# Performance work log

Hardware: AMD Instinct MI355X
Metric: run time of the kernel (lower is better)

## Reference

```python
import jax, jax.numpy as jnp
import numpy as np

N_NODES = 50000
IN_CH = 128
OUT_CH = 64
N_EDGES = 800000
K_HOPS = 2


def setup_inputs() -> dict:
    key = jax.random.key(0)
    k1, k2, k3, k4 = jax.random.split(key, 4)
    x = jax.random.normal(k1, (N_NODES, IN_CH), dtype=jnp.float32)
    edge_index = jax.random.randint(k2, (2, N_EDGES), 0, N_NODES, dtype=jnp.int64)
    # SGC linear layer params (torch Linear default init approx)
    scale = 1.0 / np.sqrt(IN_CH)
    W = jax.random.uniform(k3, (IN_CH, OUT_CH), dtype=jnp.float32, minval=-scale, maxval=scale)
    b = jax.random.uniform(k4, (OUT_CH,), dtype=jnp.float32, minval=-scale, maxval=scale)
    return {"x": x, "edge_index": edge_index, "W": W, "b": b}


def _sgc_propagate(x, row, col, K):
    # GCN symmetric normalization with self-loops: S = D^-1/2 (A+I) D^-1/2
    n = x.shape[0]
    loop = jnp.arange(n, dtype=row.dtype)
    row = jnp.concatenate([row, loop])
    col = jnp.concatenate([col, loop])
    ones = jnp.ones(row.shape[0], dtype=x.dtype)
    deg = jax.ops.segment_sum(ones, col, num_segments=n)
    dinv = jnp.where(deg > 0, jax.lax.rsqrt(deg), 0.0)
    norm = dinv[row] * dinv[col]  # [E+N]
    for _ in range(K):
        # gather source features, weight, scatter-add to targets
        msg = norm[:, None] * x[row]  # [E+N, C]
        x = jax.ops.segment_sum(msg, col, num_segments=n)
    return x


def reference(x, edge_index, W, b):
    # Dropout is identity in eval mode (deterministic reference).
    row, col = edge_index[0], edge_index[1]
    h = _sgc_propagate(x, row, col, K_HOPS)  # [N, IN_CH]
    return h @ W + b  # [N, OUT_CH]
```

## Files before the change

### kernel.cpp

```cpp
#include <hip/hip_runtime.h>

#define N_NODES 50000
#define IN_CH   128
#define OUT_CH  64
#define N_EDGES 800000
#define NBINS   49
#define LBCAP   128
#define BINCAP  20000
#define PCAP    64
#define WT_STR  136
#define SA_B    500
#define SA_E    1600
#define SB_B    49
#define GEMM_BL 196
#define HOP_NB  782
#define ZPL     (N_NODES * 4)


using short8  = __attribute__((ext_vector_type(8))) short;
using float4v = __attribute__((ext_vector_type(4))) float;
using uint4v  = __attribute__((ext_vector_type(4))) unsigned int;

__device__ __forceinline__ unsigned int bpack(float a, float b) {
    unsigned int ua = __float_as_uint(a), ub = __float_as_uint(b);
    unsigned int ra = (ua + 0x7fffu + ((ua >> 16) & 1u)) >> 16;
    unsigned int rb = (ub + 0x7fffu + ((ub >> 16) & 1u)) & 0xffff0000u;
    return (ra & 0xffffu) | rb;
}

__global__ __launch_bounds__(256) void scatter_a(const int* __restrict__ row,
        const int* __restrict__ col, unsigned int* __restrict__ binbuf,
        int* __restrict__ gcur) {
    __shared__ unsigned int sbuf[NBINS][LBCAP];
    __shared__ int scnt[NBINS];
    __shared__ int sdst[NBINS];
    const int tid = threadIdx.x;
    if (tid < NBINS) scnt[tid] = 0;
    __syncthreads();
    const int e0 = blockIdx.x * SA_E;
    for (int i = tid; i < SA_E / 4; i += 256) {
        int e = e0 + i * 4;
        int4 t4 = *(const int4*)&col[e];
        int4 s4 = *(const int4*)&row[e];
        const int ts[4] = { t4.x, t4.y, t4.z, t4.w };
        const int ss[4] = { s4.x, s4.y, s4.z, s4.w };
        #pragma unroll
        for (int j = 0; j < 4; ++j) {
            int b = ts[j] >> 10;
            int pos = atomicAdd(&scnt[b], 1);
            if (pos < LBCAP)
                sbuf[b][pos] = ((unsigned)(ts[j] & 1023) << 16) | (unsigned)ss[j];
        }
    }
    __syncthreads();
    if (tid < NBINS) {
        int c = scnt[tid]; if (c > LBCAP) c = LBCAP; scnt[tid] = c;
        sdst[tid] = atomicAdd(&gcur[tid], c);
    }
    __syncthreads();
    const int wave = tid >> 6, lane = tid & 63;
    for (int b = wave; b < NBINS; b += 4) {
        int c = scnt[b];
        size_t d = (size_t)b * BINCAP + sdst[b];
        for (int i = lane; i < c; i += 64)
            binbuf[d + i] = sbuf[b][i];
    }
}

__global__ __launch_bounds__(1024) void scatb_gemm(
        const unsigned int* __restrict__ binbuf, const int* __restrict__ gcur,
        unsigned short* __restrict__ esrc, unsigned char* __restrict__ fill8,
        const float* __restrict__ x, const float* __restrict__ W,
        float* __restrict__ y) {
    const int bid = blockIdx.x, tid = threadIdx.x;
    if (bid < SB_B) {
        __shared__ int lcnt[1024];
        const int t0 = bid << 10;
        lcnt[tid] = 0;
        __syncthreads();
        int cnt = gcur[bid]; if (cnt > BINCAP) cnt = BINCAP;
        const unsigned int* src = binbuf + (size_t)bid * BINCAP;
        for (int i = tid; i < cnt; i += 1024) {
            unsigned int e = src[i];
            int tl = e >> 16;
            int pos = atomicAdd(&lcnt[tl], 1);
            int t = t0 + tl;
            if (pos < PCAP && t < N_NODES)
                esrc[(size_t)pos * N_NODES + t] = (unsigned short)(e & 0xffffu);
        }
        __syncthreads();
        int t = t0 + tid;
        if (t < N_NODES) {
            int v = lcnt[tid]; if (v > PCAP) v = PCAP;
            fill8[t] = (unsigned char)v;
        }
        return;
    }
    __shared__ unsigned short sWT[64 * WT_STR];
    for (int i = tid; i < IN_CH * OUT_CH; i += 1024) {
        int k = i >> 6, c = i & 63;
        unsigned int u = __float_as_uint(W[i]);
        u = (u + 0x7fffu + ((u >> 16) & 1u)) >> 16;
        sWT[c * WT_STR + k] = (unsigned short)u;
    }
    __syncthreads();
    const int lane = tid & 63;
    const int quad = lane >> 4;
    const int c15  = lane & 15;
    const int tile = (bid - SB_B) * 16 + (tid >> 6);
    if (tile >= N_NODES / 16) return;

    short8 bf[4][4];
    #pragma unroll
    for (int t = 0; t < 4; ++t)
        #pragma unroll
        for (int ch = 0; ch < 4; ++ch)
            bf[ch][t] = *(const short8*)&sWT[(t * 16 + c15) * WT_STR + ch * 32 + quad * 8];

    const float* xr = x + ((size_t)tile * 16 + c15) * IN_CH;
    float4v acc[4] = {{0.f,0.f,0.f,0.f},{0.f,0.f,0.f,0.f},
                      {0.f,0.f,0.f,0.f},{0.f,0.f,0.f,0.f}};
    #pragma unroll
    for (int ch = 0; ch < 4; ++ch) {
        float4 f0 = *(const float4*)(xr + ch * 32 + quad * 8);
        float4 f1 = *(const float4*)(xr + ch * 32 + quad * 8 + 4);
        unsigned int d0 = bpack(f0.x, f0.y), d1 = bpack(f0.z, f0.w);
        unsigned int d2 = bpack(f1.x, f1.y), d3 = bpack(f1.z, f1.w);
        short8 a8;
        a8[0] = (short)d0; a8[1] = (short)(d0 >> 16);
        a8[2] = (short)d1; a8[3] = (short)(d1 >> 16);
        a8[4] = (short)d2; a8[5] = (short)(d2 >> 16);
        a8[6] = (short)d3; a8[7] = (short)(d3 >> 16);
        #pragma unroll
        for (int t = 0; t < 4; ++t)
            acc[t] = __builtin_amdgcn_mfma_f32_16x16x32_bf16(a8, bf[ch][t], acc[t], 0, 0, 0);
    }
    #pragma unroll
    for (int t = 0; t < 4; ++t)
        #pragma unroll
        for (int r = 0; r < 4; ++r)
            y[((size_t)tile * 16 + quad * 4 + r) * OUT_CH + t * 16 + c15] = acc[t][r];
}

__global__ __launch_bounds__(256) void scale_z0(const float* __restrict__ y,
        const unsigned char* __restrict__ fill8, uint4v* __restrict__ z0) {
    int gid = blockIdx.x * 256 + threadIdx.x;
    if (gid >= N_NODES * 8) return;
    int n = gid >> 3, q = gid & 7;
    int half = q >> 2, qq = q & 3;
    float d = rsqrtf((float)((int)fill8[n] + 1));
    float4 a = ((const float4*)y)[n * 16 + q * 2];
    float4 b = ((const float4*)y)[n * 16 + q * 2 + 1];
    uint4v pk;
    pk.x = bpack(d * a.x, d * a.y);
    pk.y = bpack(d * a.z, d * a.w);
    pk.z = bpack(d * b.x, d * b.y);
    pk.w = bpack(d * b.z, d * b.w);
    z0[(size_t)half * ZPL + n * 4 + qq] = pk;
}

__global__ __launch_bounds__(256) void hop_gather(const uint4v* __restrict__ hin,
        void* __restrict__ hout, const unsigned char* __restrict__ fill8,
        const unsigned short* __restrict__ esrc, const float* __restrict__ bias,
        int last) {
    const int half = blockIdx.x & 1;
    const int wg   = blockIdx.x >> 1;
    const int lane = threadIdx.x & 63;
    const int r    = lane >> 2;
    const int q    = lane & 3;
    const int t    = wg * 64 + (threadIdx.x >> 6) * 16 + r;
    if (t >= N_NODES) return;
    const int deg = fill8[t];
    const uint4v* hp = hin + (size_t)half * ZPL;

    uint4v rr = hp[t * 4 + q];
    float acc[8];
    {
        const unsigned int rw[4] = { rr.x, rr.y, rr.z, rr.w };
        #pragma unroll
        for (int j = 0; j < 4; ++j) {
            acc[2 * j]     = __uint_as_float(rw[j] << 16);
            acc[2 * j + 1] = __uint_as_float(rw[j] & 0xffff0000u);
        }
    }
    int e = 0;
    int s = (0 < deg) ? (int)esrc[t] : -1;
    while (__any(s >= 0)) {
        int sn = (e + 1 < deg) ? (int)esrc[(size_t)(e + 1) * N_NODES + t] : -1;
        if (s >= 0) {
            uint4v v = hp[s * 4 + q];
            const unsigned int rw[4] = { v.x, v.y, v.z, v.w };
            #pragma unroll
            for (int j = 0; j < 4; ++j) {
                acc[2 * j]     += __uint_as_float(rw[j] << 16);
                acc[2 * j + 1] += __uint_as_float(rw[j] & 0xffff0000u);
            }
        }
        s = sn; ++e;
    }

    if (!last) {
        float rdeg = 1.0f / (float)(deg + 1);
        uint4v pk;
        pk.x = bpack(acc[0] * rdeg, acc[1] * rdeg);
        pk.y = bpack(acc[2] * rdeg, acc[3] * rdeg);
        pk.z = bpack(acc[4] * rdeg, acc[5] * rdeg);
        pk.w = bpack(acc[6] * rdeg, acc[7] * rdeg);
        __builtin_nontemporal_store(pk,
            (uint4v*)hout + (size_t)half * ZPL + t * 4 + q);
    } else {
        float d = rsqrtf((float)(deg + 1));
        float4 b0 = ((const float4*)bias)[half * 8 + q * 2];
        float4 b1 = ((const float4*)bias)[half * 8 + q * 2 + 1];
        float4v o0 = { d * acc[0] + b0.x, d * acc[1] + b0.y,
                       d * acc[2] + b0.z, d * acc[3] + b0.w };
        float4v o1 = { d * acc[4] + b1.x, d * acc[5] + b1.y,
                       d * acc[6] + b1.z, d * acc[7] + b1.w };
        __builtin_nontemporal_store(o0, (float4v*)hout + t * 16 + half * 8 + q * 2);
        __builtin_nontemporal_store(o1, (float4v*)hout + t * 16 + half * 8 + q * 2 + 1);
    }
}

extern "C" void kernel_launch(void* const* d_in, const int* in_sizes, int n_in,
                              void* d_out, int out_size, void* d_ws, size_t ws_size,
                              hipStream_t stream) {
    const float* x  = (const float*)d_in[0];
    const int*   ei = (const int*)d_in[1];
    const float* W  = (const float*)d_in[2];
    const float* b  = (const float*)d_in[3];
    float*       out = (float*)d_out;

    const int* row = ei;
    const int* col = ei + N_EDGES;

    char* ws = (char*)d_ws;
    size_t a = 0;
    auto alloc = [&](size_t bytes) { char* p = ws + a; a = (a + bytes + 255) & ~(size_t)255; return p; };
    int*            gcur   = (int*)           alloc(NBINS * sizeof(int));
    unsigned int*   binbuf = (unsigned int*)  alloc((size_t)NBINS * BINCAP * 4);
    unsigned short* esrc   = (unsigned short*)alloc((size_t)PCAP * N_NODES * 2);
    unsigned char*  fill8  = (unsigned char*) alloc(N_NODES);
    float*          y      = (float*)         alloc((size_t)N_NODES * OUT_CH * 4);
    unsigned int*   z0     = (unsigned int*)  alloc((size_t)N_NODES * OUT_CH * 2);
    unsigned int*   z1     = (unsigned int*)  alloc((size_t)N_NODES * OUT_CH * 2);

    hipMemsetAsync(gcur, 0, NBINS * sizeof(int), stream);

    const int B = 256;
    int gS = (N_NODES * 8 + B - 1) / B;
    int gH = 2 * HOP_NB;

    scatter_a<<<SA_B, B, 0, stream>>>(row, col, binbuf, gcur);
    scatb_gemm<<<SB_B + GEMM_BL, 1024, 0, stream>>>(binbuf, gcur, esrc, fill8, x, W, y);
    scale_z0 <<<gS, B, 0, stream>>>(y, fill8, (uint4v*)z0);
    hop_gather<<<gH, B, 0, stream>>>((const uint4v*)z0, (void*)z1, fill8, esrc, b, 0);
    hop_gather<<<gH, B, 0, stream>>>((const uint4v*)z1, (void*)out, fill8, esrc, b, 1);
}
```

Measured before the change: 150.0 us.

## Fuse degree scaling into GEMM epilogue using atomic degree counts

Degrees are now counted with global atomics while the edges are binned in scatter_a. That makes the true degree available before the GEMM blocks run. The GEMM epilogue stages its output tile in shared memory, scales each row by rsqrt(deg+1), packs to bf16 and writes z0 directly with non-temporal stores. This removes the separate scale_z0 kernel and the fp32 y round trip through memory. The cost is 800k random global atomics in the binning kernel and a larger memset, and scaling now uses the uncapped degree.

```diff
diff --git a/kernel.cpp b/kernel.cpp
--- a/kernel.cpp
+++ b/kernel.cpp
@@ -15,6 +15,7 @@
 #define GEMM_BL 196
 #define HOP_NB  782
 #define ZPL     (N_NODES * 4)
+#define YT_STR  68
 
 
 using short8  = __attribute__((ext_vector_type(8))) short;
@@ -30,7 +31,7 @@
 
 __global__ __launch_bounds__(256) void scatter_a(const int* __restrict__ row,
         const int* __restrict__ col, unsigned int* __restrict__ binbuf,
-        int* __restrict__ gcur) {
+        int* __restrict__ gcur, int* __restrict__ deg32) {
     __shared__ unsigned int sbuf[NBINS][LBCAP];
     __shared__ int scnt[NBINS];
     __shared__ int sdst[NBINS];
@@ -47,6 +48,7 @@
         #pragma unroll
         for (int j = 0; j < 4; ++j) {
             int b = ts[j] >> 10;
+            atomicAdd(&deg32[ts[j]], 1);
             int pos = atomicAdd(&scnt[b], 1);
             if (pos < LBCAP)
                 sbuf[b][pos] = ((unsigned)(ts[j] & 1023) << 16) | (unsigned)ss[j];
@@ -69,9 +71,9 @@
 
 __global__ __launch_bounds__(1024) void scatb_gemm(
         const unsigned int* __restrict__ binbuf, const int* __restrict__ gcur,
-        unsigned short* __restrict__ esrc, unsigned char* __restrict__ fill8,
+        unsigned short* __restrict__ esrc, const int* __restrict__ deg32,
         const float* __restrict__ x, const float* __restrict__ W,
-        float* __restrict__ y) {
+        uint4v* __restrict__ z0) {
     const int bid = blockIdx.x, tid = threadIdx.x;
     if (bid < SB_B) {
         __shared__ int lcnt[1024];
@@ -88,15 +90,10 @@
             if (pos < PCAP && t < N_NODES)
                 esrc[(size_t)pos * N_NODES + t] = (unsigned short)(e & 0xffffu);
         }
-        __syncthreads();
-        int t = t0 + tid;
-        if (t < N_NODES) {
-            int v = lcnt[tid]; if (v > PCAP) v = PCAP;
-            fill8[t] = (unsigned char)v;
-        }
         return;
     }
     __shared__ unsigned short sWT[64 * WT_STR];
+    __shared__ float ytile[16 * 16 * YT_STR];
     for (int i = tid; i < IN_CH * OUT_CH; i += 1024) {
         int k = i >> 6, c = i & 63;
         unsigned int u = __float_as_uint(W[i]);
@@ -107,7 +104,8 @@
     const int lane = tid & 63;
     const int quad = lane >> 4;
     const int c15  = lane & 15;
-    const int tile = (bid - SB_B) * 16 + (tid >> 6);
+    const int wid  = tid >> 6;
+    const int tile = (bid - SB_B) * 16 + wid;
     if (tile >= N_NODES / 16) return;
 
     short8 bf[4][4];
@@ -135,32 +133,33 @@
         for (int t = 0; t < 4; ++t)
             acc[t] = __builtin_amdgcn_mfma_f32_16x16x32_bf16(a8, bf[ch][t], acc[t], 0, 0, 0);
     }
+    float* yt = &ytile[wid * (16 * YT_STR)];
     #pragma unroll
     for (int t = 0; t < 4; ++t)
         #pragma unroll
         for (int r = 0; r < 4; ++r)
-            y[((size_t)tile * 16 + quad * 4 + r) * OUT_CH + t * 16 + c15] = acc[t][r];
-}
-
-__global__ __launch_bounds__(256) void scale_z0(const float* __restrict__ y,
-        const unsigned char* __restrict__ fill8, uint4v* __restrict__ z0) {
-    int gid = blockIdx.x * 256 + threadIdx.x;
-    if (gid >= N_NODES * 8) return;
-    int n = gid >> 3, q = gid & 7;
-    int half = q >> 2, qq = q & 3;
-    float d = rsqrtf((float)((int)fill8[n] + 1));
-    float4 a = ((const float4*)y)[n * 16 + q * 2];
-    float4 b = ((const float4*)y)[n * 16 + q * 2 + 1];
-    uint4v pk;
-    pk.x = bpack(d * a.x, d * a.y);
-    pk.y = bpack(d * a.z, d * a.w);
-    pk.z = bpack(d * b.x, d * b.y);
-    pk.w = bpack(d * b.z, d * b.w);
-    z0[(size_t)half * ZPL + n * 4 + qq] = pk;
+            yt[(quad * 4 + r) * YT_STR + t * 16 + c15] = acc[t][r];
+    #pragma unroll
+    for (int k = 0; k < 2; ++k) {
+        int u = lane + 64 * k;
+        int node = u >> 3, j = u & 7;
+        int half = j >> 2, qq = j & 3;
+        const float* src = &yt[node * YT_STR + j * 8];
+        float4 f0 = *(const float4*)src;
+        float4 f1 = *(const float4*)(src + 4);
+        int n = tile * 16 + node;
+        float dv = rsqrtf((float)(deg32[n] + 1));
+        uint4v pk;
+        pk.x = bpack(dv * f0.x, dv * f0.y);
+        pk.y = bpack(dv * f0.z, dv * f0.w);
+        pk.z = bpack(dv * f1.x, dv * f1.y);
+        pk.w = bpack(dv * f1.z, dv * f1.w);
+        __builtin_nontemporal_store(pk, z0 + (size_t)half * ZPL + (size_t)n * 4 + qq);
+    }
 }
 
 __global__ __launch_bounds__(256) void hop_gather(const uint4v* __restrict__ hin,
-        void* __restrict__ hout, const unsigned char* __restrict__ fill8,
+        void* __restrict__ hout, const int* __restrict__ deg32,
         const unsigned short* __restrict__ esrc, const float* __restrict__ bias,
         int last) {
     const int half = blockIdx.x & 1;
@@ -170,7 +169,7 @@
     const int q    = lane & 3;
     const int t    = wg * 64 + (threadIdx.x >> 6) * 16 + r;
     if (t >= N_NODES) return;
-    const int deg = fill8[t];
+    int deg = deg32[t]; if (deg > PCAP) deg = PCAP;
     const uint4v* hp = hin + (size_t)half * ZPL;
 
     uint4v rr = hp[t * 4 + q];
@@ -237,22 +236,20 @@
     size_t a = 0;
     auto alloc = [&](size_t bytes) { char* p = ws + a; a = (a + bytes + 255) & ~(size_t)255; return p; };
     int*            gcur   = (int*)           alloc(NBINS * sizeof(int));
+    int*            deg32  = (int*)           alloc((size_t)N_NODES * sizeof(int));
     unsigned int*   binbuf = (unsigned int*)  alloc((size_t)NBINS * BINCAP * 4);
     unsigned short* esrc   = (unsigned short*)alloc((size_t)PCAP * N_NODES * 2);
-    unsigned char*  fill8  = (unsigned char*) alloc(N_NODES);
-    float*          y      = (float*)         alloc((size_t)N_NODES * OUT_CH * 4);
     unsigned int*   z0     = (unsigned int*)  alloc((size_t)N_NODES * OUT_CH * 2);
     unsigned int*   z1     = (unsigned int*)  alloc((size_t)N_NODES * OUT_CH * 2);
 
-    hipMemsetAsync(gcur, 0, NBINS * sizeof(int), stream);
+    hipMemsetAsync(gcur, 0, 256 + (size_t)N_NODES * sizeof(int), stream);
 
     const int B = 256;
-    int gS = (N_NODES * 8 + B - 1) / B;
     int gH = 2 * HOP_NB;
 
-    scatter_a<<<SA_B, B, 0, stream>>>(row, col, binbuf, gcur);
-    scatb_gemm<<<SB_B + GEMM_BL, 1024, 0, stream>>>(binbuf, gcur, esrc, fill8, x, W, y);
-    scale_z0 <<<gS, B, 0, stream>>>(y, fill8, (uint4v*)z0);
-    hop_gather<<<gH, B, 0, stream>>>((const uint4v*)z0, (void*)z1, fill8, esrc, b, 0);
-    hop_gather<<<gH, B, 0, stream>>>((const uint4v*)z1, (void*)out, fill8, esrc, b, 1);
-}
+    scatter_a<<<SA_B, B, 0, stream>>>(row, col, binbuf, gcur, deg32);
+    scatb_gemm<<<SB_B + GEMM_BL, 1024, 0, stream>>>(binbuf, gcur, esrc, deg32, x, W,
+                                                    (uint4v*)z0);
+    hop_gather<<<gH, B, 0, stream>>>((const uint4v*)z0, (void*)z1, deg32, esrc, b, 0);
+    hop_gather<<<gH, B, 0, stream>>>((const uint4v*)z1, (void*)out, deg32, esrc, b, 1);
+}
```

New measurement: 172.1 us. 14.8% more time.
